# Kernel optimization log

Hardware: AMD Instinct MI355X
Metric: run time of the kernel (lower is better)

The kernel has to match this reference:

```python
import jax, jax.numpy as jnp
import numpy as np

B, C_IN, H, W = 32, 3, 256, 256
PATCH = 16
E, C_OUT = 8, 8
C_PROJ = 16
NUM_CLASSES = 1000
SPP_LEVELS = (1, 2, 4)
GATE_STEEPNESS = 10.0


def _conv(x, w, b, pad):
    # x: [N,C,H,W], w: [O,C,kh,kw]
    y = jax.lax.conv_general_dilated(x, w, (1, 1), [(pad, pad), (pad, pad)],
                                     dimension_numbers=('NCHW', 'OIHW', 'NCHW'))
    return y + b[None, :, None, None]


def _forward(X, expert_w, expert_b, proj_w, proj_b, keys, threshold,
             final_w, final_b, lin_w, lin_b):
    Bx, C, Hx, Wx = X.shape
    h, w = Hx // PATCH, Wx // PATCH
    P = h * w
    # 1) patch extraction: [B,C,H,W] -> [B*P, C, ph, pw]
    xp = (X.reshape(Bx, C, h, PATCH, w, PATCH)
           .transpose(0, 2, 4, 1, 3, 5)
           .reshape(Bx * P, C, PATCH, PATCH))
    # 2) router: conv projection -> global avg pool -> key similarity -> softmax -> soft threshold gate
    proj = _conv(xp, proj_w, proj_b, 1)                 # [BP, 16, ph, pw]
    pooled = proj.mean(axis=(2, 3))                     # [BP, 16]
    scores = jax.nn.softmax(pooled @ keys.T, axis=-1)   # [BP, E]
    gate = scores * jax.nn.sigmoid((scores - threshold) * GATE_STEEPNESS)
    gate = gate / (gate.sum(axis=-1, keepdims=True) + 1e-9)
    gate = gate.reshape(Bx, P, E)
    # 3) all experts fused as one conv with E*C_OUT output channels (conv3x3 pad1 + ReLU)
    ew = expert_w.reshape(E * C_OUT, C, 3, 3)
    eb = expert_b.reshape(E * C_OUT)
    outs = jax.nn.relu(_conv(xp, ew, eb, 1))            # [BP, E*Cout, ph, pw]
    outs = outs.reshape(Bx, P, E, C_OUT, PATCH, PATCH)
    # 4) router-weighted combine over experts
    comb = jnp.einsum('bpe,bpeclm->bpclm', gate, outs)  # [B,P,Cout,ph,pw]
    # 5) reassemble patches -> [B, Cout, H, W]
    y = (comb.reshape(Bx, h, w, C_OUT, PATCH, PATCH)
             .transpose(0, 3, 1, 4, 2, 5)
             .reshape(Bx, C_OUT, h * PATCH, w * PATCH))
    # 6) final 1x1 conv with padding=4 (zero-pad input, bias added everywhere)
    ypad = jnp.pad(y, ((0, 0), (0, 0), (4, 4), (4, 4)))
    y = jnp.einsum('oc,bchw->bohw', final_w[:, :, 0, 0], ypad) + final_b[None, :, None, None]
    # 7) spatial pyramid pooling (levels 1,2,4) -> [B, Cout*21]
    Bc, Cc, Hc, Wc = y.shape
    feats = [y.reshape(Bc, Cc, l, Hc // l, l, Wc // l).mean(axis=(3, 5)).reshape(Bc, -1)
             for l in SPP_LEVELS]
    spp = jnp.concatenate(feats, axis=-1)
    # 8) classification head
    return spp @ lin_w + lin_b


def setup_inputs() -> dict:
    key = jax.random.key(0)
    ks = jax.random.split(key, 11)
    s = 0.1
    spp_dim = C_OUT * sum(l * l for l in SPP_LEVELS)  # 168
    return {
        'X': jax.random.normal(ks[0], (B, C_IN, H, W), jnp.float32),
        'expert_w': jax.random.normal(ks[1], (E, C_OUT, C_IN, 3, 3), jnp.float32) * s,
        'expert_b': jax.random.normal(ks[2], (E, C_OUT), jnp.float32) * s,
        'proj_w': jax.random.normal(ks[3], (C_PROJ, C_IN, 3, 3), jnp.float32) * s,
        'proj_b': jax.random.normal(ks[4], (C_PROJ,), jnp.float32) * s,
        'keys': jax.random.normal(ks[5], (E, C_PROJ), jnp.float32) * s,
        'threshold': jnp.array(0.125, jnp.float32),
        'final_w': jax.random.normal(ks[6], (C_OUT, C_OUT, 1, 1), jnp.float32) * s,
        'final_b': jax.random.normal(ks[7], (C_OUT,), jnp.float32) * s,
        'lin_w': jax.random.normal(ks[8], (spp_dim, NUM_CLASSES), jnp.float32) * s,
        'lin_b': jax.random.normal(ks[9], (NUM_CLASSES,), jnp.float32) * s,
    }


def reference(X, expert_w, expert_b, proj_w, proj_b, keys, threshold,
              final_w, final_b, lin_w, lin_b):
    return _forward(X, expert_w, expert_b, proj_w, proj_b, keys, threshold,
                    final_w, final_b, lin_w, lin_b)
```

## Files before the change

### kernel.cpp

```cpp
#include <hip/hip_runtime.h>
#include <hip/hip_bf16.h>
#include <math.h>


typedef short bf16x8 __attribute__((ext_vector_type(8)));
typedef float f32x4 __attribute__((ext_vector_type(4)));
typedef float pf2 __attribute__((ext_vector_type(2)));

__device__ __forceinline__ int cellOf(int r) {
    int rr = r + 4;
    return (rr >= 66) + (rr >= 132) + (rr >= 198);
}

__device__ __forceinline__ unsigned int packbf2(float lo, float hi) {
    __hip_bfloat162 h = __float22bfloat162_rn(make_float2(lo, hi));
    unsigned int u;
    __builtin_memcpy(&u, &h, 4);
    return u;
}

__global__ __launch_bounds__(256) void prep_kernel(
    const float* __restrict__ ew, const float* __restrict__ ebg,
    const float* __restrict__ pw, const float* __restrict__ pb,
    const float* __restrict__ keys, float* __restrict__ Sy,
    unsigned short* __restrict__ Bg, float* __restrict__ cbf)
{
    const int t = threadIdx.x;
    {
        float4* s4 = reinterpret_cast<float4*>(Sy);
        const float4 z4 = make_float4(0.f, 0.f, 0.f, 0.f);
        for (int i = t; i < 8192; i += 256) s4[i] = z4;
    }
    if (t < 72) {
        float sv[32];
        #pragma unroll
        for (int s = 0; s < 32; ++s) {
            int q, kx; bool zz = false;
            if (s < 16)       { q = s >> 1;  kx = s & 1; }
            else if (s < 18)  { q = 8;       kx = s - 16; }
            else if (s < 26)  { q = s - 18;  kx = 2; }
            else if (s == 26) { q = 8;       kx = 2; }
            else              { q = 0; kx = 0; zz = true; }
            const int ky = q / 3, c = q - ky * 3;
            const int widx = c * 9 + ky * 3 + kx;
            float a;
            if (t < 64) {
                a = ew[t * 27 + widx];
            } else {
                const int e = t - 64;
                a = 0.f;
                #pragma unroll
                for (int o = 0; o < 16; ++o)
                    a += keys[e * 16 + o] * pw[o * 27 + widx];
            }
            sv[s] = zz ? 0.f : a;
        }
        uint4 q0, q1, q2v, q3v;
        q0.x  = packbf2(sv[0],  sv[1]);  q0.y  = packbf2(sv[2],  sv[3]);
        q0.z  = packbf2(sv[4],  sv[5]);  q0.w  = packbf2(sv[6],  sv[7]);
        q1.x  = packbf2(sv[8],  sv[9]);  q1.y  = packbf2(sv[10], sv[11]);
        q1.z  = packbf2(sv[12], sv[13]); q1.w  = packbf2(sv[14], sv[15]);
        q2v.x = packbf2(sv[16], sv[17]); q2v.y = packbf2(sv[18], sv[19]);
        q2v.z = packbf2(sv[20], sv[21]); q2v.w = packbf2(sv[22], sv[23]);
        q3v.x = packbf2(sv[24], sv[25]); q3v.y = packbf2(sv[26], sv[27]);
        q3v.z = packbf2(sv[28], sv[29]); q3v.w = packbf2(sv[30], sv[31]);
        uint4* dst = reinterpret_cast<uint4*>(&Bg[t * 32]);
        dst[0] = q0; dst[1] = q1; dst[2] = q2v; dst[3] = q3v;
    }
    if (t >= 128 && t < 208) {
        const int i = t - 128;
        float c;
        if (i < 64) {
            c = ebg[i];
        } else {
            const int e = (i - 64) & 7;
            c = 0.f;
            #pragma unroll
            for (int o = 0; o < 16; ++o) c += keys[e * 16 + o] * pb[o];
        }
        cbf[i] = c;
    }
}

#define MFMA_CORE(PKV, ACCJ) do {                                           \
    const bf16x8 afr = __builtin_bit_cast(bf16x8, (PKV));                   \
    const f32x4 a0 = __builtin_amdgcn_mfma_f32_16x16x32_bf16(afr, bfr0, cbv0, 0, 0, 0); \
    const f32x4 a1 = __builtin_amdgcn_mfma_f32_16x16x32_bf16(afr, bfr1, cbv1, 0, 0, 0); \
    const f32x4 a2 = __builtin_amdgcn_mfma_f32_16x16x32_bf16(afr, bfr2, cbv2, 0, 0, 0); \
    const f32x4 a3 = __builtin_amdgcn_mfma_f32_16x16x32_bf16(afr, bfr3, cbv3, 0, 0, 0); \
    a4acc = __builtin_amdgcn_mfma_f32_16x16x32_bf16(afr, bfr4, a4acc, 0, 0, 0); \
    const pf2 z2_ = {0.f, 0.f};                                             \
    {                                                                       \
        const pf2 l_ = __builtin_elementwise_max((pf2)__builtin_shufflevector(a0, a0, 0, 1), z2_); \
        const pf2 h_ = __builtin_elementwise_max((pf2)__builtin_shufflevector(a0, a0, 2, 3), z2_); \
        pall2[0] += l_ + h_;                                                \
        if (ACCJ) psb2[0] += l_ * jm2lo + h_ * jm2hi;                       \
    }                                                                       \
    {                                                                       \
        const pf2 l_ = __builtin_elementwise_max((pf2)__builtin_shufflevector(a1, a1, 0, 1), z2_); \
        const pf2 h_ = __builtin_elementwise_max((pf2)__builtin_shufflevector(a1, a1, 2, 3), z2_); \
        pall2[1] += l_ + h_;                                                \
        if (ACCJ) psb2[1] += l_ * jm2lo + h_ * jm2hi;                       \
    }                                                                       \
    {                                                                       \
        const pf2 l_ = __builtin_elementwise_max((pf2)__builtin_shufflevector(a2, a2, 0, 1), z2_); \
        const pf2 h_ = __builtin_elementwise_max((pf2)__builtin_shufflevector(a2, a2, 2, 3), z2_); \
        pall2[2] += l_ + h_;                                                \
        if (ACCJ) psb2[2] += l_ * jm2lo + h_ * jm2hi;                       \
    }                                                                       \
    {                                                                       \
        const pf2 l_ = __builtin_elementwise_max((pf2)__builtin_shufflevector(a3, a3, 0, 1), z2_); \
        const pf2 h_ = __builtin_elementwise_max((pf2)__builtin_shufflevector(a3, a3, 2, 3), z2_); \
        pall2[3] += l_ + h_;                                                \
        if (ACCJ) psb2[3] += l_ * jm2lo + h_ * jm2hi;                       \
    }                                                                       \
} while (0)

#define CONV_STEP_L(SB) do {                                                \
    uint4 pkv;                                                              \
    pkv.x = pkw[offp0 + (SB)];                                              \
    pkv.y = pkw[offp1 + (SB)];                                              \
    pkv.z = pkw[offp2 + (SB)];                                              \
    pkv.w = pkw[offp3 + (SB)];                                              \
    MFMA_CORE(pkv, 1);                                                      \
} while (0)

#define GATES_FROM_RSUM()                                                   \
    rsum += __shfl_xor(rsum, 16);                                           \
    rsum += __shfl_xor(rsum, 32);                                           \
    float gv[4];                                                            \
    {                                                                       \
        float lg = rsum * (1.f / 256.f);                                    \
        float mx = fmaxf(lg, __shfl_xor(lg, 1));                            \
        mx = fmaxf(mx, __shfl_xor(mx, 2));                                  \
        mx = fmaxf(mx, __shfl_xor(mx, 4));                                  \
        float ex = __expf(lg - mx);                                         \
        float s = ex;                                                       \
        s += __shfl_xor(s, 1); s += __shfl_xor(s, 2); s += __shfl_xor(s, 4);\
        float sc = ex / s;                                                  \
        float g = sc / (1.f + __expf(-(sc - thr) * 10.f));                  \
        float gs = g;                                                       \
        gs += __shfl_xor(gs, 1); gs += __shfl_xor(gs, 2); gs += __shfl_xor(gs, 4); \
        float gn = g / (gs + 1e-9f);                                        \
        const int gb = (lid & 56);                                          \
        const int hb = (lid >> 3) & 1;                                      \
        gv[0] = __shfl(gn, gb | (0 + hb));                                  \
        gv[1] = __shfl(gn, gb | (2 + hb));                                  \
        gv[2] = __shfl(gn, gb | (4 + hb));                                  \
        gv[3] = __shfl(gn, gb | (6 + hb));                                  \
    }

__global__ __launch_bounds__(256, 3) void fused_kernel(
    const float* __restrict__ X, const unsigned short* __restrict__ Bg,
    const float* __restrict__ thr_p, const float* __restrict__ cbf,
    float* __restrict__ Sy)
{
    __shared__ __align__(16) unsigned int pk[4][1952];

    const int t = threadIdx.x;
    const int wid = t >> 6, lid = t & 63;
    const int r16 = lid & 15, kb = lid >> 4;

    const int wgid = blockIdx.x;
    const int virt = (wgid & 7) * 256 + (wgid >> 3);

    const int gp = (virt << 2) + wid;
    const int b = gp >> 8;
    const int pi = (gp >> 4) & 15, pj = gp & 15;
    const int rbase = pi << 4, cbase = pj << 4;

    unsigned int* pkw = pk[wid];
    const float thr = thr_p[0];

    const int lr = lid >> 2, lq = lid & 3;
    const float* xb = X + ((b * 3) << 16) + ((rbase + lr) << 8) + cbase + (lq << 2);
    const float4 xv0 = *reinterpret_cast<const float4*>(xb);
    const float4 xv1 = *reinterpret_cast<const float4*>(xb + 65536);
    const float4 xv2 = *reinterpret_cast<const float4*>(xb + 131072);

    const bf16x8 bfr0 = *reinterpret_cast<const bf16x8*>(&Bg[(r16) * 32 + (kb << 3)]);
    const bf16x8 bfr1 = *reinterpret_cast<const bf16x8*>(&Bg[(16 + r16) * 32 + (kb << 3)]);
    const bf16x8 bfr2 = *reinterpret_cast<const bf16x8*>(&Bg[(32 + r16) * 32 + (kb << 3)]);
    const bf16x8 bfr3 = *reinterpret_cast<const bf16x8*>(&Bg[(48 + r16) * 32 + (kb << 3)]);
    const bf16x8 bfr4 = *reinterpret_cast<const bf16x8*>(&Bg[(64 + (r16 & 7)) * 32 + (kb << 3)]);

    const float cbs0 = cbf[r16];
    const float cbs1 = cbf[16 + r16];
    const float cbs2 = cbf[32 + r16];
    const float cbs3 = cbf[48 + r16];
    const float cbs4 = cbf[64 + r16];

    if (lid < 54) {
        pkw[lid] = 0u;
        pkw[918 + lid] = 0u;
        pkw[976 + lid] = 0u;
        pkw[1894 + lid] = 0u;
    }
    if (lid < 48) {
        const int y3 = lid / 3;
        const int cp = lid - y3 * 3;
        pkw[976 + (y3 + 1) * 54 + cp * 18 + 16] = 0u;
    }
    __builtin_amdgcn_wave_barrier();

    float s0 = __shfl_up(xv0.w, 1);
    float s1 = __shfl_up(xv1.w, 1);
    float s2 = __shfl_up(xv2.w, 1);
    const float c0p = (lq == 0) ? 0.f : s0;
    const float c1p = (lq == 0) ? 0.f : s1;
    const float c2p = (lq == 0) ? 0.f : s2;
    float nxx = __shfl_down(xv0.x, 4);
    float nxy = __shfl_down(xv0.y, 4);
    float nxz = __shfl_down(xv0.z, 4);
    float nxw = __shfl_down(xv0.w, 4);
    if (lr == 15) { nxx = 0.f; nxy = 0.f; nxz = 0.f; nxw = 0.f; }

    {
        const int y = lr + 1;
        const int b2 = y * 54 + (lq << 2);
        unsigned int u0, u1, u2, u3;
        u0 = packbf2(c0p,   xv0.x); u1 = packbf2(xv0.x, xv0.y);
        u2 = packbf2(xv0.y, xv0.z); u3 = packbf2(xv0.z, xv0.w);
        *reinterpret_cast<uint2*>(&pkw[b2])      = make_uint2(u0, u1);
        *reinterpret_cast<uint2*>(&pkw[b2 + 2])  = make_uint2(u2, u3);
        u0 = packbf2(c1p,   xv1.x); u1 = packbf2(xv1.x, xv1.y);
        u2 = packbf2(xv1.y, xv1.z); u3 = packbf2(xv1.z, xv1.w);
        *reinterpret_cast<uint2*>(&pkw[b2 + 18]) = make_uint2(u0, u1);
        *reinterpret_cast<uint2*>(&pkw[b2 + 20]) = make_uint2(u2, u3);
        u0 = packbf2(c2p,   xv2.x); u1 = packbf2(xv2.x, xv2.y);
        u2 = packbf2(xv2.y, xv2.z); u3 = packbf2(xv2.z, xv2.w);
        *reinterpret_cast<uint2*>(&pkw[b2 + 36]) = make_uint2(u0, u1);
        *reinterpret_cast<uint2*>(&pkw[b2 + 38]) = make_uint2(u2, u3);

        const int bx = 976 + y * 54 + (lq << 2);
        u0 = packbf2(xv0.x, xv1.x); u1 = packbf2(xv0.y, xv1.y);
        u2 = packbf2(xv0.z, xv1.z); u3 = packbf2(xv0.w, xv1.w);
        *reinterpret_cast<uint2*>(&pkw[bx])      = make_uint2(u0, u1);
        *reinterpret_cast<uint2*>(&pkw[bx + 2])  = make_uint2(u2, u3);
        u0 = packbf2(xv1.x, xv2.x); u1 = packbf2(xv1.y, xv2.y);
        u2 = packbf2(xv1.z, xv2.z); u3 = packbf2(xv1.w, xv2.w);
        *reinterpret_cast<uint2*>(&pkw[bx + 18]) = make_uint2(u0, u1);
        *reinterpret_cast<uint2*>(&pkw[bx + 20]) = make_uint2(u2, u3);
        u0 = packbf2(xv2.x, nxx);  u1 = packbf2(xv2.y, nxy);
        u2 = packbf2(xv2.z, nxz);  u3 = packbf2(xv2.w, nxw);
        *reinterpret_cast<uint2*>(&pkw[bx + 36]) = make_uint2(u0, u1);
        *reinterpret_cast<uint2*>(&pkw[bx + 38]) = make_uint2(u2, u3);

        if (lr == 0) {
            const int b0 = 976 + 36 + (lq << 2);
            u0 = packbf2(0.f, xv0.x); u1 = packbf2(0.f, xv0.y);
            u2 = packbf2(0.f, xv0.z); u3 = packbf2(0.f, xv0.w);
            *reinterpret_cast<uint2*>(&pkw[b0])     = make_uint2(u0, u1);
            *reinterpret_cast<uint2*>(&pkw[b0 + 2]) = make_uint2(u2, u3);
        }
    }
    __builtin_amdgcn_wave_barrier();

    int offp0, offp1, offp2, offp3;
    if (kb < 2) {
        const int t0 = kb * 72 + r16;
        offp0 = t0; offp1 = t0 + 18; offp2 = t0 + 36; offp3 = t0 + 54;
    } else if (kb == 2) {
        offp0 = 144 + r16; offp1 = 977 + r16; offp2 = 1013 + r16; offp3 = 1049 + r16;
    } else {
        offp0 = 1085 + r16; offp1 = 1121 + r16; offp2 = 1121 + r16; offp3 = 1121 + r16;
    }

    const f32x4 cbv0 = {cbs0, cbs0, cbs0, cbs0};
    const f32x4 cbv1 = {cbs1, cbs1, cbs1, cbs1};
    const f32x4 cbv2 = {cbs2, cbs2, cbs2, cbs2};
    const f32x4 cbv3 = {cbs3, cbs3, cbs3, cbs3};
    const float rb16 = cbs4 * 16.f;
    f32x4 a4acc = {rb16, rb16, rb16, rb16};

    const int iA = cellOf(rbase), iB = cellOf(rbase + 15);
    const int jA = cellOf(cbase), jB = cellOf(cbase + 15);
    const int isp = (iA + 1) * 66 - 4 - rbase;
    const int jsp = (jA + 1) * 66 - 4 - cbase;
    const bool anySplit = (isp < 16) | (jsp < 16);

    const int slot = ((pi & 1) << 1) | (pj & 1);
    const int lbase = (b << 6) + (slot << 4);
    const pf2 zz2 = {0.f, 0.f};

    if (!anySplit) {
        unsigned int rg[16][4];
        #pragma unroll
        for (int mt = 0; mt < 16; ++mt) {
            rg[mt][0] = pkw[offp0 + mt * 54];
            rg[mt][1] = pkw[offp1 + mt * 54];
            rg[mt][2] = pkw[offp2 + mt * 54];
            rg[mt][3] = pkw[offp3 + mt * 54];
        }

        pf2 pall2[4] = {zz2, zz2, zz2, zz2};
        pf2 psb2[4]  = {zz2, zz2, zz2, zz2};
        pf2 jm2lo = zz2, jm2hi = zz2;
        #pragma unroll
        for (int mt = 0; mt < 16; ++mt) {
            uint4 pkv;
            pkv.x = rg[mt][0]; pkv.y = rg[mt][1];
            pkv.z = rg[mt][2]; pkv.w = rg[mt][3];
            MFMA_CORE(pkv, 0);
        }

        float rsum = (a4acc[0] + a4acc[1]) + (a4acc[2] + a4acc[3]);
        GATES_FROM_RSUM();

        float tt = 0.f;
        #pragma unroll
        for (int nt = 0; nt < 4; ++nt)
            tt = fmaf(gv[nt], pall2[nt].x + pall2[nt].y, tt);
        tt += __shfl_xor(tt, 8);
        tt += __shfl_xor(tt, 16);
        tt += __shfl_xor(tt, 32);
        if (lid < 8)
            atomicAdd(&Sy[(iA * 4 + jA) * 2048 + lbase + lid], tt);
    } else {
        float jmask[4];
        #pragma unroll
        for (int r = 0; r < 4; ++r)
            jmask[r] = ((kb << 2) + r >= jsp) ? 1.f : 0.f;
        const pf2 jm2lo = {jmask[0], jmask[1]};
        const pf2 jm2hi = {jmask[2], jmask[3]};

        pf2 pall2[4] = {zz2, zz2, zz2, zz2};
        pf2 psb2[4]  = {zz2, zz2, zz2, zz2};
        const int m1 = isp < 16 ? isp : 16;

        int sb = 0;
        for (int mt = 0; mt < m1; ++mt) { CONV_STEP_L(sb); sb += 54; }
        const float pa0_0 = pall2[0].x + pall2[0].y;
        const float pa0_1 = pall2[1].x + pall2[1].y;
        const float pa0_2 = pall2[2].x + pall2[2].y;
        const float pa0_3 = pall2[3].x + pall2[3].y;
        const float pb0_0 = psb2[0].x + psb2[0].y;
        const float pb0_1 = psb2[1].x + psb2[1].y;
        const float pb0_2 = psb2[2].x + psb2[2].y;
        const float pb0_3 = psb2[3].x + psb2[3].y;
        pall2[0] = pall2[1] = pall2[2] = pall2[3] = zz2;
        psb2[0] = psb2[1] = psb2[2] = psb2[3] = zz2;
        for (int mt = m1; mt < 16; ++mt) { CONV_STEP_L(sb); sb += 54; }

        float rsum = (a4acc[0] + a4acc[1]) + (a4acc[2] + a4acc[3]);
        GATES_FROM_RSUM();

        float tTA = gv[0] * pa0_0 + gv[1] * pa0_1 + gv[2] * pa0_2 + gv[3] * pa0_3;
        float tTB = gv[0] * pb0_0 + gv[1] * pb0_1 + gv[2] * pb0_2 + gv[3] * pb0_3;
        float tBA = 0.f, tBB = 0.f;
        #pragma unroll
        for (int nt = 0; nt < 4; ++nt) {
            tBA = fmaf(gv[nt], pall2[nt].x + pall2[nt].y, tBA);
            tBB = fmaf(gv[nt], psb2[nt].x + psb2[nt].y, tBB);
        }
        #pragma unroll
        for (int m = 8; m <= 32; m <<= 1) {
            tTA += __shfl_xor(tTA, m);
            tTB += __shfl_xor(tTB, m);
            tBA += __shfl_xor(tBA, m);
            tBB += __shfl_xor(tBB, m);
        }
        if (lid < 8) {
            atomicAdd(&Sy[(iA * 4 + jA) * 2048 + lbase + lid], tTA - tTB);
            atomicAdd(&Sy[(iA * 4 + jB) * 2048 + lbase + lid], tTB);
            atomicAdd(&Sy[(iB * 4 + jA) * 2048 + lbase + lid], tBA - tBB);
            atomicAdd(&Sy[(iB * 4 + jB) * 2048 + lbase + lid], tBB);
        }
    }
}

__global__ __launch_bounds__(256) void head_kernel(
    const float* __restrict__ Sy, const float* __restrict__ fw,
    const float* __restrict__ fb, const float* __restrict__ lw,
    const float* __restrict__ lb, float* __restrict__ out)
{
    __shared__ float syl[128];
    __shared__ float s2[32];
    __shared__ float stot[8];
    __shared__ float spp[168];
    const int t = threadIdx.x;
    const int b = blockIdx.y;
    if (t < 128) {
        const int c = t >> 4, cell = t & 15;
        const float* p = &Sy[cell * 2048 + (b << 6) + c];
        syl[t] = (p[0] + p[16]) + (p[32] + p[48]);
    }
    __syncthreads();
    if (t < 32) {
        int c = t >> 2, I = (t >> 1) & 1, J = t & 1;
        const float* p = &syl[c * 16];
        s2[t] = p[(2 * I) * 4 + 2 * J] + p[(2 * I) * 4 + 2 * J + 1] +
                p[(2 * I + 1) * 4 + 2 * J] + p[(2 * I + 1) * 4 + 2 * J + 1];
    } else if (t >= 32 && t < 40) {
        int c = t - 32;
        float s = 0.f;
        #pragma unroll
        for (int i2 = 0; i2 < 16; ++i2) s += syl[c * 16 + i2];
        stot[c] = s;
    }
    __syncthreads();
    if (t < 168) {
        float acc = 0.f;
        int o;
        if (t < 8) {
            o = t;
            #pragma unroll
            for (int c = 0; c < 8; ++c) acc += fw[o * 8 + c] * stot[c];
            acc *= (1.f / 69696.f);
        } else if (t < 40) {
            int m = t - 8; o = m >> 2; int q = m & 3;
            #pragma unroll
            for (int c = 0; c < 8; ++c) acc += fw[o * 8 + c] * s2[c * 4 + q];
            acc *= (1.f / 17424.f);
        } else {
            int m = t - 40; o = m >> 4; int cell = m & 15;
            #pragma unroll
            for (int c = 0; c < 8; ++c) acc += fw[o * 8 + c] * syl[c * 16 + cell];
            acc *= (1.f / 4356.f);
        }
        spp[t] = acc + fb[o];
    }
    __syncthreads();
    const int n = blockIdx.x * 256 + t;
    if (n < 1000) {
        float acc = lb[n];
        for (int k = 0; k < 168; ++k) acc = fmaf(spp[k], lw[k * 1000 + n], acc);
        out[b * 1000 + n] = acc;
    }
}

extern "C" void kernel_launch(void* const* d_in, const int* in_sizes, int n_in,
                              void* d_out, int out_size, void* d_ws, size_t ws_size,
                              hipStream_t stream) {
    const float* X    = (const float*)d_in[0];
    const float* ew   = (const float*)d_in[1];
    const float* eb   = (const float*)d_in[2];
    const float* pw   = (const float*)d_in[3];
    const float* pb   = (const float*)d_in[4];
    const float* keys = (const float*)d_in[5];
    const float* thr  = (const float*)d_in[6];
    const float* fw   = (const float*)d_in[7];
    const float* fb   = (const float*)d_in[8];
    const float* lw   = (const float*)d_in[9];
    const float* lb   = (const float*)d_in[10];
    float* out = (float*)d_out;
    float* Sy  = (float*)d_ws;
    unsigned short* Bg = (unsigned short*)((float*)d_ws + 32768);
    float* cbf = (float*)d_ws + 33920;

    prep_kernel<<<1, 256, 0, stream>>>(ew, eb, pw, pb, keys, Sy, Bg, cbf);
    fused_kernel<<<2048, 256, 0, stream>>>(X, Bg, thr, cbf, Sy);
    head_kernel<<<dim3(4, 32), 256, 0, stream>>>(Sy, fw, fb, lw, lb, out);
}
```

Measured before the change: 38.06 us.

## Process two patches per wave with software-prefetched input for the next patch

Each wave now handles two patches in sequence, halving the grid to 1024 blocks. It issues the global loads for the second patch's input right after staging the first patch into shared memory, so load latency overlaps the first patch's MFMA conv work. It also drops the explicit register staging of all 16 LDS fragments in the non-split path and reads them directly per step. Launch bounds drop to 2 blocks per CU, trading occupancy for more registers and intra-wave overlap.

```diff
diff --git a/kernel.cpp b/kernel.cpp
--- a/kernel.cpp
+++ b/kernel.cpp
@@ -116,6 +116,15 @@
     }                                                                       \
 } while (0)
 
+#define CONV_STEP_N(SB) do {                                                \
+    uint4 pkv;                                                              \
+    pkv.x = pkw[offp0 + (SB)];                                              \
+    pkv.y = pkw[offp1 + (SB)];                                              \
+    pkv.z = pkw[offp2 + (SB)];                                              \
+    pkv.w = pkw[offp3 + (SB)];                                              \
+    MFMA_CORE(pkv, 0);                                                      \
+} while (0)
+
 #define CONV_STEP_L(SB) do {                                                \
     uint4 pkv;                                                              \
     pkv.x = pkw[offp0 + (SB)];                                              \
@@ -150,7 +159,7 @@
         gv[3] = __shfl(gn, gb | (6 + hb));                                  \
     }
 
-__global__ __launch_bounds__(256, 3) void fused_kernel(
+__global__ __launch_bounds__(256, 2) void fused_kernel(
     const float* __restrict__ X, const unsigned short* __restrict__ Bg,
     const float* __restrict__ thr_p, const float* __restrict__ cbf,
     float* __restrict__ Sy)
@@ -162,21 +171,11 @@
     const int r16 = lid & 15, kb = lid >> 4;
 
     const int wgid = blockIdx.x;
-    const int virt = (wgid & 7) * 256 + (wgid >> 3);
-
-    const int gp = (virt << 2) + wid;
-    const int b = gp >> 8;
-    const int pi = (gp >> 4) & 15, pj = gp & 15;
-    const int rbase = pi << 4, cbase = pj << 4;
+    const int virt = (wgid & 7) * 128 + (wgid >> 3);
+    const int g0 = (virt << 2) + wid;
 
     unsigned int* pkw = pk[wid];
     const float thr = thr_p[0];
-
-    const int lr = lid >> 2, lq = lid & 3;
-    const float* xb = X + ((b * 3) << 16) + ((rbase + lr) << 8) + cbase + (lq << 2);
-    const float4 xv0 = *reinterpret_cast<const float4*>(xb);
-    const float4 xv1 = *reinterpret_cast<const float4*>(xb + 65536);
-    const float4 xv2 = *reinterpret_cast<const float4*>(xb + 131072);
 
     const bf16x8 bfr0 = *reinterpret_cast<const bf16x8*>(&Bg[(r16) * 32 + (kb << 3)]);
     const bf16x8 bfr1 = *reinterpret_cast<const bf16x8*>(&Bg[(16 + r16) * 32 + (kb << 3)]);
@@ -189,72 +188,11 @@
     const float cbs2 = cbf[32 + r16];
     const float cbs3 = cbf[48 + r16];
     const float cbs4 = cbf[64 + r16];
-
-    if (lid < 54) {
-        pkw[lid] = 0u;
-        pkw[918 + lid] = 0u;
-        pkw[976 + lid] = 0u;
-        pkw[1894 + lid] = 0u;
-    }
-    if (lid < 48) {
-        const int y3 = lid / 3;
-        const int cp = lid - y3 * 3;
-        pkw[976 + (y3 + 1) * 54 + cp * 18 + 16] = 0u;
-    }
-    __builtin_amdgcn_wave_barrier();
-
-    float s0 = __shfl_up(xv0.w, 1);
-    float s1 = __shfl_up(xv1.w, 1);
-    float s2 = __shfl_up(xv2.w, 1);
-    const float c0p = (lq == 0) ? 0.f : s0;
-    const float c1p = (lq == 0) ? 0.f : s1;
-    const float c2p = (lq == 0) ? 0.f : s2;
-    float nxx = __shfl_down(xv0.x, 4);
-    float nxy = __shfl_down(xv0.y, 4);
-    float nxz = __shfl_down(xv0.z, 4);
-    float nxw = __shfl_down(xv0.w, 4);
-    if (lr == 15) { nxx = 0.f; nxy = 0.f; nxz = 0.f; nxw = 0.f; }
-
-    {
-        const int y = lr + 1;
-        const int b2 = y * 54 + (lq << 2);
-        unsigned int u0, u1, u2, u3;
-        u0 = packbf2(c0p,   xv0.x); u1 = packbf2(xv0.x, xv0.y);
-        u2 = packbf2(xv0.y, xv0.z); u3 = packbf2(xv0.z, xv0.w);
-        *reinterpret_cast<uint2*>(&pkw[b2])      = make_uint2(u0, u1);
-        *reinterpret_cast<uint2*>(&pkw[b2 + 2])  = make_uint2(u2, u3);
-        u0 = packbf2(c1p,   xv1.x); u1 = packbf2(xv1.x, xv1.y);
-        u2 = packbf2(xv1.y, xv1.z); u3 = packbf2(xv1.z, xv1.w);
-        *reinterpret_cast<uint2*>(&pkw[b2 + 18]) = make_uint2(u0, u1);
-        *reinterpret_cast<uint2*>(&pkw[b2 + 20]) = make_uint2(u2, u3);
-        u0 = packbf2(c2p,   xv2.x); u1 = packbf2(xv2.x, xv2.y);
-        u2 = packbf2(xv2.y, xv2.z); u3 = packbf2(xv2.z, xv2.w);
-        *reinterpret_cast<uint2*>(&pkw[b2 + 36]) = make_uint2(u0, u1);
-        *reinterpret_cast<uint2*>(&pkw[b2 + 38]) = make_uint2(u2, u3);
-
-        const int bx = 976 + y * 54 + (lq << 2);
-        u0 = packbf2(xv0.x, xv1.x); u1 = packbf2(xv0.y, xv1.y);
-        u2 = packbf2(xv0.z, xv1.z); u3 = packbf2(xv0.w, xv1.w);
-        *reinterpret_cast<uint2*>(&pkw[bx])      = make_uint2(u0, u1);
-        *reinterpret_cast<uint2*>(&pkw[bx + 2])  = make_uint2(u2, u3);
-        u0 = packbf2(xv1.x, xv2.x); u1 = packbf2(xv1.y, xv2.y);
-        u2 = packbf2(xv1.z, xv2.z); u3 = packbf2(xv1.w, xv2.w);
-        *reinterpret_cast<uint2*>(&pkw[bx + 18]) = make_uint2(u0, u1);
-        *reinterpret_cast<uint2*>(&pkw[bx + 20]) = make_uint2(u2, u3);
-        u0 = packbf2(xv2.x, nxx);  u1 = packbf2(xv2.y, nxy);
-        u2 = packbf2(xv2.z, nxz);  u3 = packbf2(xv2.w, nxw);
-        *reinterpret_cast<uint2*>(&pkw[bx + 36]) = make_uint2(u0, u1);
-        *reinterpret_cast<uint2*>(&pkw[bx + 38]) = make_uint2(u2, u3);
-
-        if (lr == 0) {
-            const int b0 = 976 + 36 + (lq << 2);
-            u0 = packbf2(0.f, xv0.x); u1 = packbf2(0.f, xv0.y);
-            u2 = packbf2(0.f, xv0.z); u3 = packbf2(0.f, xv0.w);
-            *reinterpret_cast<uint2*>(&pkw[b0])     = make_uint2(u0, u1);
-            *reinterpret_cast<uint2*>(&pkw[b0 + 2]) = make_uint2(u2, u3);
-        }
-    }
-    __builtin_amdgcn_wave_barrier();
+    const f32x4 cbv0 = {cbs0, cbs0, cbs0, cbs0};
+    const f32x4 cbv1 = {cbs1, cbs1, cbs1, cbs1};
+    const f32x4 cbv2 = {cbs2, cbs2, cbs2, cbs2};
+    const f32x4 cbv3 = {cbs3, cbs3, cbs3, cbs3};
+    const float rb16 = cbs4 * 16.f;
 
     int offp0, offp1, offp2, offp3;
     if (kb < 2) {
@@ -266,106 +204,187 @@
         offp0 = 1085 + r16; offp1 = 1121 + r16; offp2 = 1121 + r16; offp3 = 1121 + r16;
     }
 
-    const f32x4 cbv0 = {cbs0, cbs0, cbs0, cbs0};
-    const f32x4 cbv1 = {cbs1, cbs1, cbs1, cbs1};
-    const f32x4 cbv2 = {cbs2, cbs2, cbs2, cbs2};
-    const f32x4 cbv3 = {cbs3, cbs3, cbs3, cbs3};
-    const float rb16 = cbs4 * 16.f;
-    f32x4 a4acc = {rb16, rb16, rb16, rb16};
-
-    const int iA = cellOf(rbase), iB = cellOf(rbase + 15);
-    const int jA = cellOf(cbase), jB = cellOf(cbase + 15);
-    const int isp = (iA + 1) * 66 - 4 - rbase;
-    const int jsp = (jA + 1) * 66 - 4 - cbase;
-    const bool anySplit = (isp < 16) | (jsp < 16);
-
-    const int slot = ((pi & 1) << 1) | (pj & 1);
-    const int lbase = (b << 6) + (slot << 4);
-    const pf2 zz2 = {0.f, 0.f};
-
-    if (!anySplit) {
-        unsigned int rg[16][4];
-        #pragma unroll
-        for (int mt = 0; mt < 16; ++mt) {
-            rg[mt][0] = pkw[offp0 + mt * 54];
-            rg[mt][1] = pkw[offp1 + mt * 54];
-            rg[mt][2] = pkw[offp2 + mt * 54];
-            rg[mt][3] = pkw[offp3 + mt * 54];
-        }
-
-        pf2 pall2[4] = {zz2, zz2, zz2, zz2};
-        pf2 psb2[4]  = {zz2, zz2, zz2, zz2};
-        pf2 jm2lo = zz2, jm2hi = zz2;
-        #pragma unroll
-        for (int mt = 0; mt < 16; ++mt) {
-            uint4 pkv;
-            pkv.x = rg[mt][0]; pkv.y = rg[mt][1];
-            pkv.z = rg[mt][2]; pkv.w = rg[mt][3];
-            MFMA_CORE(pkv, 0);
-        }
-
-        float rsum = (a4acc[0] + a4acc[1]) + (a4acc[2] + a4acc[3]);
-        GATES_FROM_RSUM();
-
-        float tt = 0.f;
-        #pragma unroll
-        for (int nt = 0; nt < 4; ++nt)
-            tt = fmaf(gv[nt], pall2[nt].x + pall2[nt].y, tt);
-        tt += __shfl_xor(tt, 8);
-        tt += __shfl_xor(tt, 16);
-        tt += __shfl_xor(tt, 32);
-        if (lid < 8)
-            atomicAdd(&Sy[(iA * 4 + jA) * 2048 + lbase + lid], tt);
-    } else {
-        float jmask[4];
-        #pragma unroll
-        for (int r = 0; r < 4; ++r)
-            jmask[r] = ((kb << 2) + r >= jsp) ? 1.f : 0.f;
-        const pf2 jm2lo = {jmask[0], jmask[1]};
-        const pf2 jm2hi = {jmask[2], jmask[3]};
-
-        pf2 pall2[4] = {zz2, zz2, zz2, zz2};
-        pf2 psb2[4]  = {zz2, zz2, zz2, zz2};
-        const int m1 = isp < 16 ? isp : 16;
-
-        int sb = 0;
-        for (int mt = 0; mt < m1; ++mt) { CONV_STEP_L(sb); sb += 54; }
-        const float pa0_0 = pall2[0].x + pall2[0].y;
-        const float pa0_1 = pall2[1].x + pall2[1].y;
-        const float pa0_2 = pall2[2].x + pall2[2].y;
-        const float pa0_3 = pall2[3].x + pall2[3].y;
-        const float pb0_0 = psb2[0].x + psb2[0].y;
-        const float pb0_1 = psb2[1].x + psb2[1].y;
-        const float pb0_2 = psb2[2].x + psb2[2].y;
-        const float pb0_3 = psb2[3].x + psb2[3].y;
-        pall2[0] = pall2[1] = pall2[2] = pall2[3] = zz2;
-        psb2[0] = psb2[1] = psb2[2] = psb2[3] = zz2;
-        for (int mt = m1; mt < 16; ++mt) { CONV_STEP_L(sb); sb += 54; }
-
-        float rsum = (a4acc[0] + a4acc[1]) + (a4acc[2] + a4acc[3]);
-        GATES_FROM_RSUM();
-
-        float tTA = gv[0] * pa0_0 + gv[1] * pa0_1 + gv[2] * pa0_2 + gv[3] * pa0_3;
-        float tTB = gv[0] * pb0_0 + gv[1] * pb0_1 + gv[2] * pb0_2 + gv[3] * pb0_3;
-        float tBA = 0.f, tBB = 0.f;
-        #pragma unroll
-        for (int nt = 0; nt < 4; ++nt) {
-            tBA = fmaf(gv[nt], pall2[nt].x + pall2[nt].y, tBA);
-            tBB = fmaf(gv[nt], psb2[nt].x + psb2[nt].y, tBB);
-        }
-        #pragma unroll
-        for (int m = 8; m <= 32; m <<= 1) {
-            tTA += __shfl_xor(tTA, m);
-            tTB += __shfl_xor(tTB, m);
-            tBA += __shfl_xor(tBA, m);
-            tBB += __shfl_xor(tBB, m);
-        }
-        if (lid < 8) {
-            atomicAdd(&Sy[(iA * 4 + jA) * 2048 + lbase + lid], tTA - tTB);
-            atomicAdd(&Sy[(iA * 4 + jB) * 2048 + lbase + lid], tTB);
-            atomicAdd(&Sy[(iB * 4 + jA) * 2048 + lbase + lid], tBA - tBB);
-            atomicAdd(&Sy[(iB * 4 + jB) * 2048 + lbase + lid], tBB);
-        }
+    const int lr = lid >> 2, lq = lid & 3;
+
+    if (lid < 54) {
+        pkw[lid] = 0u;
+        pkw[918 + lid] = 0u;
+        pkw[976 + lid] = 0u;
+        pkw[1894 + lid] = 0u;
+    }
+    if (lid < 48) {
+        const int y3 = lid / 3;
+        const int cp = lid - y3 * 3;
+        pkw[976 + (y3 + 1) * 54 + cp * 18 + 16] = 0u;
+    }
+    __builtin_amdgcn_wave_barrier();
+
+    float4 c0, c1, c2;
+    {
+        const int b = g0 >> 8;
+        const int rb = ((g0 >> 4) & 15) << 4, cb = (g0 & 15) << 4;
+        const float* xb = X + ((b * 3) << 16) + ((rb + lr) << 8) + cb + (lq << 2);
+        c0 = *reinterpret_cast<const float4*>(xb);
+        c1 = *reinterpret_cast<const float4*>(xb + 65536);
+        c2 = *reinterpret_cast<const float4*>(xb + 131072);
+    }
+
+    float4 n0, n1, n2;
+    #pragma unroll
+    for (int pp = 0; pp < 2; ++pp) {
+        const int gp = g0 | (pp << 12);
+        const int b = gp >> 8;
+        const int pi = (gp >> 4) & 15, pj = gp & 15;
+        const int rbase = pi << 4, cbase = pj << 4;
+
+        float s0 = __shfl_up(c0.w, 1);
+        float s1 = __shfl_up(c1.w, 1);
+        float s2 = __shfl_up(c2.w, 1);
+        const float c0p = (lq == 0) ? 0.f : s0;
+        const float c1p = (lq == 0) ? 0.f : s1;
+        const float c2p = (lq == 0) ? 0.f : s2;
+        float nxx = __shfl_down(c0.x, 4);
+        float nxy = __shfl_down(c0.y, 4);
+        float nxz = __shfl_down(c0.z, 4);
+        float nxw = __shfl_down(c0.w, 4);
+        if (lr == 15) { nxx = 0.f; nxy = 0.f; nxz = 0.f; nxw = 0.f; }
+
+        {
+            const int y = lr + 1;
+            const int b2 = y * 54 + (lq << 2);
+            unsigned int u0, u1, u2, u3;
+            u0 = packbf2(c0p,  c0.x); u1 = packbf2(c0.x, c0.y);
+            u2 = packbf2(c0.y, c0.z); u3 = packbf2(c0.z, c0.w);
+            *reinterpret_cast<uint2*>(&pkw[b2])      = make_uint2(u0, u1);
+            *reinterpret_cast<uint2*>(&pkw[b2 + 2])  = make_uint2(u2, u3);
+            u0 = packbf2(c1p,  c1.x); u1 = packbf2(c1.x, c1.y);
+            u2 = packbf2(c1.y, c1.z); u3 = packbf2(c1.z, c1.w);
+            *reinterpret_cast<uint2*>(&pkw[b2 + 18]) = make_uint2(u0, u1);
+            *reinterpret_cast<uint2*>(&pkw[b2 + 20]) = make_uint2(u2, u3);
+            u0 = packbf2(c2p,  c2.x); u1 = packbf2(c2.x, c2.y);
+            u2 = packbf2(c2.y, c2.z); u3 = packbf2(c2.z, c2.w);
+            *reinterpret_cast<uint2*>(&pkw[b2 + 36]) = make_uint2(u0, u1);
+            *reinterpret_cast<uint2*>(&pkw[b2 + 38]) = make_uint2(u2, u3);
+
+            const int bx = 976 + y * 54 + (lq << 2);
+            u0 = packbf2(c0.x, c1.x); u1 = packbf2(c0.y, c1.y);
+            u2 = packbf2(c0.z, c1.z); u3 = packbf2(c0.w, c1.w);
+            *reinterpret_cast<uint2*>(&pkw[bx])      = make_uint2(u0, u1);
+            *reinterpret_cast<uint2*>(&pkw[bx + 2])  = make_uint2(u2, u3);
+            u0 = packbf2(c1.x, c2.x); u1 = packbf2(c1.y, c2.y);
+            u2 = packbf2(c1.z, c2.z); u3 = packbf2(c1.w, c2.w);
+            *reinterpret_cast<uint2*>(&pkw[bx + 18]) = make_uint2(u0, u1);
+            *reinterpret_cast<uint2*>(&pkw[bx + 20]) = make_uint2(u2, u3);
+            u0 = packbf2(c2.x, nxx);  u1 = packbf2(c2.y, nxy);
+            u2 = packbf2(c2.z, nxz);  u3 = packbf2(c2.w, nxw);
+            *reinterpret_cast<uint2*>(&pkw[bx + 36]) = make_uint2(u0, u1);
+            *reinterpret_cast<uint2*>(&pkw[bx + 38]) = make_uint2(u2, u3);
+
+            if (lr == 0) {
+                const int b0 = 976 + 36 + (lq << 2);
+                u0 = packbf2(0.f, c0.x); u1 = packbf2(0.f, c0.y);
+                u2 = packbf2(0.f, c0.z); u3 = packbf2(0.f, c0.w);
+                *reinterpret_cast<uint2*>(&pkw[b0])     = make_uint2(u0, u1);
+                *reinterpret_cast<uint2*>(&pkw[b0 + 2]) = make_uint2(u2, u3);
+            }
+        }
+        __builtin_amdgcn_wave_barrier();
+
+        if (pp == 0) {
+            const int gq = g0 | 4096;
+            const int b2 = gq >> 8;
+            const int rb2 = ((gq >> 4) & 15) << 4, cb2 = (gq & 15) << 4;
+            const float* xb2 = X + ((b2 * 3) << 16) + ((rb2 + lr) << 8) + cb2 + (lq << 2);
+            n0 = *reinterpret_cast<const float4*>(xb2);
+            n1 = *reinterpret_cast<const float4*>(xb2 + 65536);
+            n2 = *reinterpret_cast<const float4*>(xb2 + 131072);
+        }
+
+        const int iA = cellOf(rbase), iB = cellOf(rbase + 15);
+        const int jA = cellOf(cbase), jB = cellOf(cbase + 15);
+        const int isp = (iA + 1) * 66 - 4 - rbase;
+        const int jsp = (jA + 1) * 66 - 4 - cbase;
+        const bool anySplit = (isp < 16) | (jsp < 16);
+
+        const int slot = ((pi & 1) << 1) | (pj & 1);
+        const int lbase = (b << 6) + (slot << 4);
+        const pf2 zz2 = {0.f, 0.f};
+        f32x4 a4acc = {rb16, rb16, rb16, rb16};
+
+        if (!anySplit) {
+            pf2 pall2[4] = {zz2, zz2, zz2, zz2};
+            pf2 psb2[4]  = {zz2, zz2, zz2, zz2};
+            pf2 jm2lo = zz2, jm2hi = zz2;
+            (void)psb2; (void)jm2lo; (void)jm2hi;
+            #pragma unroll
+            for (int mt = 0; mt < 16; ++mt) CONV_STEP_N(mt * 54);
+
+            float rsum = (a4acc[0] + a4acc[1]) + (a4acc[2] + a4acc[3]);
+            GATES_FROM_RSUM();
+
+            float tt = 0.f;
+            #pragma unroll
+            for (int nt = 0; nt < 4; ++nt)
+                tt = fmaf(gv[nt], pall2[nt].x + pall2[nt].y, tt);
+            tt += __shfl_xor(tt, 8);
+            tt += __shfl_xor(tt, 16);
+            tt += __shfl_xor(tt, 32);
+            if (lid < 8)
+                atomicAdd(&Sy[(iA * 4 + jA) * 2048 + lbase + lid], tt);
+        } else {
+            float jmask[4];
+            #pragma unroll
+            for (int r = 0; r < 4; ++r)
+                jmask[r] = ((kb << 2) + r >= jsp) ? 1.f : 0.f;
+            const pf2 jm2lo = {jmask[0], jmask[1]};
+            const pf2 jm2hi = {jmask[2], jmask[3]};
+
+            pf2 pall2[4] = {zz2, zz2, zz2, zz2};
+            pf2 psb2[4]  = {zz2, zz2, zz2, zz2};
+            const int m1 = isp < 16 ? isp : 16;
+
+            int sb = 0;
+            for (int mt = 0; mt < m1; ++mt) { CONV_STEP_L(sb); sb += 54; }
+            const float pa0_0 = pall2[0].x + pall2[0].y;
+            const float pa0_1 = pall2[1].x + pall2[1].y;
+            const float pa0_2 = pall2[2].x + pall2[2].y;
+            const float pa0_3 = pall2[3].x + pall2[3].y;
+            const float pb0_0 = psb2[0].x + psb2[0].y;
+            const float pb0_1 = psb2[1].x + psb2[1].y;
+            const float pb0_2 = psb2[2].x + psb2[2].y;
+            const float pb0_3 = psb2[3].x + psb2[3].y;
+            pall2[0] = pall2[1] = pall2[2] = pall2[3] = zz2;
+            psb2[0] = psb2[1] = psb2[2] = psb2[3] = zz2;
+            for (int mt = m1; mt < 16; ++mt) { CONV_STEP_L(sb); sb += 54; }
+
+            float rsum = (a4acc[0] + a4acc[1]) + (a4acc[2] + a4acc[3]);
+            GATES_FROM_RSUM();
+
+            float tTA = gv[0] * pa0_0 + gv[1] * pa0_1 + gv[2] * pa0_2 + gv[3] * pa0_3;
+            float tTB = gv[0] * pb0_0 + gv[1] * pb0_1 + gv[2] * pb0_2 + gv[3] * pb0_3;
+            float tBA = 0.f, tBB = 0.f;
+            #pragma unroll
+            for (int nt = 0; nt < 4; ++nt) {
+                tBA = fmaf(gv[nt], pall2[nt].x + pall2[nt].y, tBA);
+                tBB = fmaf(gv[nt], psb2[nt].x + psb2[nt].y, tBB);
+            }
+            #pragma unroll
+            for (int m = 8; m <= 32; m <<= 1) {
+                tTA += __shfl_xor(tTA, m);
+                tTB += __shfl_xor(tTB, m);
+                tBA += __shfl_xor(tBA, m);
+                tBB += __shfl_xor(tBB, m);
+            }
+            if (lid < 8) {
+                atomicAdd(&Sy[(iA * 4 + jA) * 2048 + lbase + lid], tTA - tTB);
+                atomicAdd(&Sy[(iA * 4 + jB) * 2048 + lbase + lid], tTB);
+                atomicAdd(&Sy[(iB * 4 + jA) * 2048 + lbase + lid], tBA - tBB);
+                atomicAdd(&Sy[(iB * 4 + jB) * 2048 + lbase + lid], tBB);
+            }
+        }
+
+        if (pp == 0) { c0 = n0; c1 = n1; c2 = n2; }
+        __builtin_amdgcn_wave_barrier();
     }
 }
 
@@ -449,6 +468,6 @@
     float* cbf = (float*)d_ws + 33920;
 
     prep_kernel<<<1, 256, 0, stream>>>(ew, eb, pw, pb, keys, Sy, Bg, cbf);
-    fused_kernel<<<2048, 256, 0, stream>>>(X, Bg, thr, cbf, Sy);
+    fused_kernel<<<1024, 256, 0, stream>>>(X, Bg, thr, cbf, Sy);
     head_kernel<<<dim3(4, 32), 256, 0, stream>>>(Sy, fw, fb, lw, lb, out);
 }
```

New measurement: 41.07 us. +7.9%, slower.
